# Optimization experiments

Measured on AMD Instinct MI355X. Metric: run time of the kernel, lower is better.

## Reference

```python
import jax, jax.numpy as jnp
import numpy as np

B, T, I, H, C, S, V = 32, 64, 300, 168, 168, 512, 50257


def setup_inputs() -> dict:
    key = jax.random.key(0)
    ks = jax.random.split(key, 10)
    s = 0.05
    return {
        "x": jax.random.normal(ks[0], (B, T, I), jnp.float32),
        "context": jax.random.normal(ks[1], (B, S, C), jnp.float32),
        "context_lengths": jax.random.randint(ks[2], (B,), 1, S + 1),
        "W_ih": jax.random.normal(ks[3], (4 * H, I + C), jnp.float32) * s,
        "W_hh": jax.random.normal(ks[4], (4 * H, H), jnp.float32) * s,
        "b_ih": jnp.zeros((4 * H,), jnp.float32),
        "b_hh": jnp.zeros((4 * H,), jnp.float32),
        "att_Wx": jax.random.normal(ks[5], (H, H), jnp.float32) * s,
        "att_Ws": jax.random.normal(ks[6], (C, H), jnp.float32) * s,
        "att_b": jnp.zeros((H,), jnp.float32),
        "att_v": jax.random.normal(ks[7], (H,), jnp.float32) * s,
        "W_dec": jax.random.normal(ks[8], (V, H), jnp.float32) * s,
    }


def reference(x, context, context_lengths, W_ih, W_hh, b_ih, b_hh,
              att_Wx, att_Ws, att_b, att_v, W_dec):
    # x: (B, T, I); context: (B, S, C)
    b, t, _ = x.shape
    s_len = context.shape[1]
    h_dim = W_hh.shape[1]
    dtype = x.dtype

    # valid-position mask for attention over source context
    mask = jnp.arange(s_len)[None, :] < context_lengths[:, None]  # (B, S)
    # seq projection is time-invariant: precompute once outside the step loop
    seq_proj = jnp.einsum('bsc,ca->bsa', context, att_Ws)  # (B, S, H)

    h0 = jnp.zeros((b, h_dim), dtype)
    c0 = jnp.zeros((b, h_dim), dtype)

    def step(carry, x_t):
        h, c = carry
        # MLP (additive) attention: v . tanh(Wx h + Ws seq + b)
        e = jnp.einsum('bsa,a->bs',
                       jnp.tanh((h @ att_Wx)[:, None, :] + seq_proj + att_b),
                       att_v)  # (B, S)
        e = jnp.where(mask, e, jnp.asarray(-1e9, dtype))
        w = jax.nn.softmax(e, axis=-1)
        attn_ctx = jnp.einsum('bs,bsc->bc', w, context)  # (B, C)

        # concat input with attended context, single-layer LSTM cell
        rnn_in = jnp.concatenate([x_t, attn_ctx], axis=1)  # (B, I+C)
        gates = rnn_in @ W_ih.T + b_ih + h @ W_hh.T + b_hh  # (B, 4H)
        i_g, f_g, g_g, o_g = jnp.split(gates, 4, axis=1)    # torch ifgo order
        c_new = jax.nn.sigmoid(f_g) * c + jax.nn.sigmoid(i_g) * jnp.tanh(g_g)
        h_new = jax.nn.sigmoid(o_g) * jnp.tanh(c_new)

        dec = h_new @ W_dec.T  # (B, V), bias-free decode
        return (h_new, c_new), dec

    _, decs = jax.lax.scan(step, (h0, c0), jnp.swapaxes(x, 0, 1))  # (T, B, V)
    return jnp.swapaxes(decs, 0, 1)  # (B, T, V)
```

## Files before the change

### kernel.cpp

```cpp
#include <hip/hip_runtime.h>
#include <stdint.h>

#define BB 32
#define TT 64
#define ID 300
#define HH 168
#define SS 512
#define VV 50257
#define G4 672
#define IC 468
#define KP 192
#define NP2 50432
#define NJ 8
#define RPB 21
#define CPB 84
#define KK 336
#define WKP 88
#define EPAD 170
#define SBLK 64
#define LSLOT 192
#define HROW 96
#define LP 72
#define NTN 197
#define NTILES 1576

typedef float f32x4 __attribute__((ext_vector_type(4)));
typedef short bf16x8 __attribute__((ext_vector_type(8)));
typedef unsigned long long u64;

__device__ __forceinline__ float bf2f(unsigned short u) {
  union { unsigned int i; float f; } v; v.i = ((unsigned int)u) << 16; return v.f;
}
__device__ __forceinline__ unsigned short f2bf(float f) {
  union { float f; unsigned int u; } v; v.f = f;
  unsigned int r = v.u + 0x7fffu + ((v.u >> 16) & 1u);
  return (unsigned short)(r >> 16);
}
__device__ __forceinline__ float rcpf(float x) { return __builtin_amdgcn_rcpf(x); }
__device__ __forceinline__ u64 packft(float f, unsigned tag) {
  union { float f; unsigned u; } v; v.f = f;
  return ((u64)tag << 32) | (u64)v.u;
}
__device__ __forceinline__ float lo_f(u64 x) {
  union { unsigned u; float f; } v; v.u = (unsigned)x; return v.f;
}
__device__ __forceinline__ unsigned hi_u(u64 x) { return (unsigned)(x >> 32); }
__device__ __forceinline__ void postv(u64* p, u64 v) {
  __hip_atomic_store(p, v, __ATOMIC_RELAXED, __HIP_MEMORY_SCOPE_AGENT);
}
__device__ __forceinline__ u64 loadv(const u64* p) {
  return __hip_atomic_load(p, __ATOMIC_RELAXED, __HIP_MEMORY_SCOPE_AGENT);
}
__device__ __forceinline__ void postu(unsigned* p, unsigned v) {
  __hip_atomic_store(p, v, __ATOMIC_RELAXED, __HIP_MEMORY_SCOPE_AGENT);
}
__device__ __forceinline__ unsigned loadu(const unsigned* p) {
  return __hip_atomic_load(p, __ATOMIC_RELAXED, __HIP_MEMORY_SCOPE_AGENT);
}

#define NB_WDEC 4728
#define NB_TR   788
__global__ void k_prepall(const float* __restrict__ Wih, const float* __restrict__ Whh,
                          const float* __restrict__ attWx, const float* __restrict__ Wd,
                          float* __restrict__ WihxT, unsigned short* __restrict__ Wdb,
                          float* __restrict__ WgT, unsigned short* __restrict__ WxS,
                          u64* __restrict__ Abuf, u64* __restrict__ Pbuf,
                          unsigned* __restrict__ pw) {
  const int bid = blockIdx.x, tid = threadIdx.x;
  if (bid < NB_WDEC) {
    size_t e0 = ((size_t)bid * 256 + tid) * 8;
    int v = (int)(e0 / KP), kp0 = (int)(e0 - (size_t)v * KP);
    int rg = kp0 / 24, off0 = kp0 - rg * 24;
    unsigned short o[8];
    if (v < VV) {
      const float* src = Wd + (size_t)v * HH + rg * RPB + off0;
      #pragma unroll
      for (int i = 0; i < 8; ++i) o[i] = (off0 + i < RPB) ? f2bf(src[i]) : 0;
    } else {
      #pragma unroll
      for (int i = 0; i < 8; ++i) o[i] = 0;
    }
    *(uint4*)(Wdb + e0) = *(const uint4*)o;
    return;
  }
  if (bid < NB_WDEC + NB_TR) {
    int idx = (bid - NB_WDEC) * 256 + tid;
    if (idx < ID * G4) {
      int k = idx / G4, i = idx - k * G4;
      WihxT[idx] = Wih[(size_t)i * IC + k];
    }
    return;
  }
  int idx = (bid - NB_WDEC - NB_TR) * 256 + tid;
  const int T1 = NJ * KK * WKP;
  const int T2 = T1 + NJ * RPB * HH;
  const int ZH = BB * NJ * LSLOT;
  const int T3 = T2 + 2 * ZH + 64;
  if (idx < T1) {
    int j = idx / (KK * WKP); int r = idx - j * (KK * WKP);
    int k = r / WKP, col = r - k * WKP;
    float w = 0.f;
    if (col < CPB) {
      int gt = col / RPB, rr = col - gt * RPB;
      int gcol = gt * HH + j * RPB + rr;
      w = (k < HH) ? Wih[(size_t)gcol * IC + ID + k] : Whh[(size_t)gcol * HH + (k - HH)];
    }
    WgT[idx] = w;
  } else if (idx < T2) {
    int r = idx - T1;
    WxS[r] = f2bf(attWx[r]);
  } else if (idx < T3) {
    int r = idx - T2;
    if (r < ZH) Abuf[r] = 0ull;
    else if (r < 2 * ZH) Pbuf[r - ZH] = 0ull;
    else pw[r - 2 * ZH] = 0u;
  }
}

__global__ void k_seqxp(const float* __restrict__ ctx, const float* __restrict__ Ws,
                        const float* __restrict__ x, const float* __restrict__ WihxT,
                        const float* __restrict__ bih, const float* __restrict__ bhh,
                        unsigned short* __restrict__ ETs, unsigned short* __restrict__ ctxb,
                        float* __restrict__ Xp) {
  __shared__ float sbuf[2688];
  const int tid = threadIdx.x;
  if (blockIdx.x < 1024) {
    const int b = blockIdx.x & 31;
    const int s0 = (blockIdx.x >> 5) * 16;
    for (int idx = tid; idx < 16 * HH; idx += 256) {
      float v = ctx[(size_t)(b * SS + s0) * HH + idx];
      sbuf[idx] = v;
      ctxb[(size_t)(b * SS + s0) * HH + idx] = f2bf(v);
    }
    __syncthreads();
    #pragma unroll
    for (int o = 0; o < 11; ++o) {
      int idx = o * 256 + tid;
      if (idx < 16 * HH) {
        int s = idx / HH, h = idx - s * HH;
        const float* cr = &sbuf[s * HH];
        float acc = 0.f;
        #pragma unroll 4
        for (int c = 0; c < HH; ++c) acc = fmaf(cr[c], Ws[c * HH + h], acc);
        ETs[(size_t)(b * SS + s0 + s) * HH + h] = f2bf(__expf(2.f * acc));
      }
    }
  } else {
    const int r = blockIdx.x - 1024;
    const int t0 = (r & 7) * 8;
    const int b = r >> 3;
    for (int idx = tid; idx < 8 * ID; idx += 256)
      sbuf[idx] = x[(size_t)(b * TT + t0) * ID + idx];
    __syncthreads();
    for (int i = tid; i < G4; i += 256) {
      float bias = bih[i] + bhh[i];
      float acc[8];
      #pragma unroll
      for (int tt = 0; tt < 8; ++tt) acc[tt] = bias;
      for (int k = 0; k < ID; ++k) {
        float w = WihxT[k * G4 + i];
        #pragma unroll
        for (int tt = 0; tt < 8; ++tt) acc[tt] += sbuf[tt * ID + k] * w;
      }
      #pragma unroll
      for (int tt = 0; tt < 8; ++tt)
        Xp[(size_t)(b * TT + t0 + tt) * G4 + i] = acc[tt];
    }
  }
}

__global__ __launch_bounds__(512, 1) void k_recur(
    const int* __restrict__ lens, const float* __restrict__ attb,
    const float* __restrict__ attv, const float* __restrict__ WgT,
    const unsigned short* __restrict__ WxS, const unsigned short* __restrict__ ETs,
    const unsigned short* __restrict__ ctxb, const float* __restrict__ Xp,
    u64* __restrict__ Abuf, u64* __restrict__ Pbuf,
    unsigned* __restrict__ hallA, const unsigned short* __restrict__ Wdb,
    float* __restrict__ out, unsigned* __restrict__ pw) {
  const int b = blockIdx.x & 31;
  const int j = blockIdx.x >> 5;
  const int tid = threadIdx.x;

  __shared__ __align__(16) float WgL[KK][WKP];
  __shared__ unsigned short EL[SBLK][EPAD];
  __shared__ unsigned short WxL[RPB][HH];
  __shared__ float scratch[512];
  __shared__ float redH[504], redC[504];
  __shared__ float gE[HH], hsh[HH], abL[HH], vL[HH], attn[HH];
  __shared__ float esh[SBLK], hLoc[RPB], cLoc[RPB], wsum[8];
  __shared__ float sumv_s, bsum_s;
  __shared__ int sClaim;

  {
    const f32x4* src = (const f32x4*)(WgT + (size_t)j * KK * WKP);
    f32x4* dst = (f32x4*)WgL;
    for (int i = tid; i < KK * WKP / 4; i += 512) dst[i] = src[i];
  }
  for (int i = tid; i < SBLK * HH; i += 512) {
    int s = i / HH, h = i - s * HH;
    EL[s][h] = ETs[((size_t)b * SS + j * SBLK + s) * HH + h];
  }
  for (int i = tid; i < RPB * HH; i += 512)
    ((unsigned short*)WxL)[i] = WxS[(size_t)j * RPB * HH + i];
  if (tid < HH) { abL[tid] = attb[tid]; vL[tid] = attv[tid]; }
  if (tid < RPB) cLoc[tid] = 0.f;
  __syncthreads();
  if (tid == 0) {
    float s = 0.f;
    for (int h = 0; h < HH; ++h) s += vL[h];
    sumv_s = s;
  }
  const int len = lens[b];
  const int sbase = j * SBLK;
  u64* Amine = Abuf + (size_t)(b * NJ + j) * LSLOT;
  u64* Pmine = Pbuf + (size_t)(b * NJ + j) * LSLOT;
  __syncthreads();

  for (int t = 0; t < TT; ++t) {
    float xa0=0,xa1=0,xa2=0,xa3=0, xb0=0,xb1=0,xb2=0,xb3=0;
    if (tid < 11) {
      const float* xp = Xp + ((size_t)b * TT + t) * G4 + j * RPB;
      int r0 = 2 * tid, r1 = r0 + 1;
      xa0 = xp[r0]; xa1 = xp[HH + r0]; xa2 = xp[2*HH + r0]; xa3 = xp[3*HH + r0];
      if (r1 < RPB) { xb0 = xp[r1]; xb1 = xp[HH + r1]; xb2 = xp[2*HH + r1]; xb3 = xp[3*HH + r1]; }
    }
    if (tid < HH) {
      float a = abL[tid], hv = 0.f;
      if (t > 0) {
        const unsigned want = (unsigned)t;
        const int jh = tid / RPB, hr = tid - jh * RPB;
        u64 va[9];
        int g = 0;
        for (;;) {
          #pragma unroll
          for (int jj = 0; jj < NJ; ++jj)
            va[jj] = loadv(&Abuf[(size_t)(b * NJ + jj) * LSLOT + tid]);
          va[8] = loadv(&Abuf[(size_t)(b * NJ + jh) * LSLOT + HH + hr]);
          bool ok = true;
          #pragma unroll
          for (int q = 0; q < 9; ++q) ok &= (hi_u(va[q]) >= want);
          if (ok) break;
          __builtin_amdgcn_s_sleep(1);
          if (++g > (1 << 24)) break;
        }
        #pragma unroll
        for (int jj = 0; jj < NJ; ++jj) a += lo_f(va[jj]);
        hv = lo_f(va[8]);
      }
      gE[tid] = __expf(2.f * a);
      hsh[tid] = hv;
    }
    __syncthreads();
    {
      int w = tid >> 6, lane = tid & 63;
      int sl = w * 8 + (lane >> 3);
      int hg = lane & 7;
      const unsigned short* er = &EL[sl][hg * RPB];
      const int hb = hg * RPB;
      float ep = 0.f;
      #pragma unroll 7
      for (int i = 0; i < RPB; ++i)
        ep += vL[hb + i] * rcpf(fmaf(gE[hb + i], bf2f(er[i]), 1.f));
      ep += __shfl_xor(ep, 1); ep += __shfl_xor(ep, 2); ep += __shfl_xor(ep, 4);
      float eh = (sbase + sl < len) ? __expf(sumv_s - 2.f * ep) : 0.f;
      float ws = (hg == 0) ? eh : 0.f;
      ws += __shfl_xor(ws, 8); ws += __shfl_xor(ws, 16); ws += __shfl_xor(ws, 32);
      if (lane == 0) wsum[w] = ws;
      if (hg == 0) esh[sl] = eh;
    }
    __syncthreads();
    if (tid < 504) {
      int c = tid % HH, ch = tid / HH;
      const unsigned short* cb = ctxb + ((size_t)b * SS + sbase) * HH + c;
      float p = 0.f;
      for (int s = ch; s < SBLK; s += 3)
        p = fmaf(esh[s], bf2f(cb[(size_t)s * HH]), p);
      scratch[ch * HH + c] = p;
    } else if (tid == 504) {
      float bs = 0.f;
      #pragma unroll
      for (int w = 0; w < 8; ++w) bs += wsum[w];
      bsum_s = bs;
    }
    __syncthreads();
    if (tid < HH) {
      float p = scratch[tid] + scratch[HH + tid] + scratch[2 * HH + tid];
      postv(&Pmine[tid], packft(p, (unsigned)(t + 1)));
    } else if (tid == HH) {
      postv(&Pmine[HH], packft(bsum_s, (unsigned)(t + 1)));
    }
    if (tid < 504) {
      int col = tid % CPB, kc = tid / CPB;
      int k0 = HH + kc * 28;
      float acc = 0.f;
      #pragma unroll 7
      for (int i = 0; i < 28; ++i)
        acc = fmaf(WgL[k0 + i][col], hsh[kc * 28 + i], acc);
      redH[kc * CPB + col] = acc;
    }
    if (tid < HH) {
      const unsigned want = (unsigned)(t + 1);
      u64 pv[NJ], bv[NJ];
      int g = 0;
      for (;;) {
        #pragma unroll
        for (int jj = 0; jj < NJ; ++jj) {
          const u64* pb = Pbuf + (size_t)(b * NJ + jj) * LSLOT;
          pv[jj] = loadv(&pb[tid]);
          bv[jj] = loadv(&pb[HH]);
        }
        bool ok = true;
        #pragma unroll
        for (int jj = 0; jj < NJ; ++jj) ok &= (hi_u(pv[jj]) >= want) & (hi_u(bv[jj]) >= want);
        if (ok) break;
        __builtin_amdgcn_s_sleep(1);
        if (++g > (1 << 24)) break;
      }
      float s = 0.f, den = 0.f;
      #pragma unroll
      for (int jj = 0; jj < NJ; ++jj) { s += lo_f(pv[jj]); den += lo_f(bv[jj]); }
      attn[tid] = s * rcpf(den);
    }
    __syncthreads();
    if (tid < 504) {
      int col = tid % CPB, kc = tid / CPB;
      int k0 = kc * 28;
      float acc = 0.f;
      #pragma unroll 7
      for (int i = 0; i < 28; ++i)
        acc = fmaf(WgL[k0 + i][col], attn[k0 + i], acc);
      redC[kc * CPB + col] = acc;
    }
    __syncthreads();
    if (tid < 12) {
      size_t hrow = ((size_t)b * TT + t) * HROW + j * 12;
      if (tid < 11) {
        const int r0 = 2 * tid, r1 = r0 + 1;
        float g0 = xa0, g1 = xa1, g2 = xa2, g3 = xa3;
        #pragma unroll
        for (int kc = 0; kc < 6; ++kc) {
          const float* rh = &redH[kc * CPB];
          const float* rc = &redC[kc * CPB];
          g0 += rh[r0] + rc[r0];
          g1 += rh[RPB + r0] + rc[RPB + r0];
          g2 += rh[2 * RPB + r0] + rc[2 * RPB + r0];
          g3 += rh[3 * RPB + r0] + rc[3 * RPB + r0];
        }
        float si = rcpf(1.f + __expf(-g0));
        float sf = rcpf(1.f + __expf(-g1));
        float tg = 1.f - 2.f * rcpf(1.f + __expf(2.f * g2));
        float so = rcpf(1.f + __expf(-g3));
        float cn = fmaf(sf, cLoc[r0], si * tg);
        float tc = 1.f - 2.f * rcpf(1.f + __expf(2.f * cn));
        float h0 = so * tc;
        cLoc[r0] = cn; hLoc[r0] = h0;
        unsigned hv = (unsigned)f2bf(h0);
        if (r1 < RPB) {
          float G0 = xb0, G1 = xb1, G2 = xb2, G3 = xb3;
          #pragma unroll
          for (int kc = 0; kc < 6; ++kc) {
            const float* rh = &redH[kc * CPB];
            const float* rc = &redC[kc * CPB];
            G0 += rh[r1] + rc[r1];
            G1 += rh[RPB + r1] + rc[RPB + r1];
            G2 += rh[2 * RPB + r1] + rc[2 * RPB + r1];
            G3 += rh[3 * RPB + r1] + rc[3 * RPB + r1];
          }
          float Si = rcpf(1.f + __expf(-G0));
          float Sf = rcpf(1.f + __expf(-G1));
          float Tg = 1.f - 2.f * rcpf(1.f + __expf(2.f * G2));
          float So = rcpf(1.f + __expf(-G3));
          float Cn = fmaf(Sf, cLoc[r1], Si * Tg);
          float Tc = 1.f - 2.f * rcpf(1.f + __expf(2.f * Cn));
          float h1 = So * Tc;
          cLoc[r1] = Cn; hLoc[r1] = h1;
          hv |= ((unsigned)f2bf(h1)) << 16;
        }
        postu(&hallA[hrow + tid], hv);
      } else {
        postu(&hallA[hrow + 11], 0u);
      }
    }
    __syncthreads();
    if (tid < HH) {
      float acc = 0.f;
      #pragma unroll
      for (int r = 0; r < RPB; ++r)
        acc = fmaf(hLoc[r], bf2f(WxL[r][tid]), acc);
      postv(&Amine[tid], packft(acc, (unsigned)(t + 1)));
    } else if (tid < HH + RPB) {
      postv(&Amine[tid], packft(hLoc[tid - HH], (unsigned)(t + 1)));
    }
  }

  __syncthreads();
  if (tid == 0) {
    __hip_atomic_fetch_add(&pw[0], 1u, __ATOMIC_RELAXED, __HIP_MEMORY_SCOPE_AGENT);
    int g = 0;
    while (loadu(&pw[0]) < (unsigned)(BB * NJ)) {
      __builtin_amdgcn_s_sleep(2);
      if (++g > (1 << 26)) break;
    }
  }
  __syncthreads();

  unsigned short* As = (unsigned short*)&WgL[0][0];
  unsigned short* Bs = As + 256 * LP;
  for (;;) {
    if (tid == 0) {
      unsigned w = __hip_atomic_fetch_add(&pw[32], 1u, __ATOMIC_RELAXED,
                                          __HIP_MEMORY_SCOPE_AGENT);
      sClaim = (w < NTILES) ? (int)w : -1;
    }
    __syncthreads();
    const int w = sClaim;
    if (w < 0) break;
    const int mt = w / NTN, nt = w - mt * NTN;
    const int m0 = mt * 256, n0 = nt * 256;
    const int lane = tid & 63, wid = tid >> 6;
    const int wm = wid >> 2, wn = wid & 3;
    const int lr = lane & 15, lk = lane >> 4;
    f32x4 acc[8][4];
    #pragma unroll
    for (int i = 0; i < 8; ++i)
      #pragma unroll
      for (int jj = 0; jj < 4; ++jj) acc[i][jj] = (f32x4)0.f;
    for (int k0 = 0; k0 < KP; k0 += 64) {
      if (k0) __syncthreads();
      #pragma unroll
      for (int i = 0; i < 4; ++i) {
        int flat = i * 512 + tid;
        int row = flat >> 3;
        int c8 = flat & 7;
        uint4 va = *(const uint4*)(hallA + (size_t)(m0 + row) * HROW + k0 / 2 + c8 * 4);
        *(uint4*)&As[row * LP + c8 * 8] = va;
        uint4 vb = *(const uint4*)(Wdb + (size_t)(n0 + row) * KP + k0 + c8 * 8);
        *(uint4*)&Bs[row * LP + c8 * 8] = vb;
      }
      __syncthreads();
      #pragma unroll
      for (int kk = 0; kk < 64; kk += 32) {
        bf16x8 af[8], bfr[4];
        #pragma unroll
        for (int mi = 0; mi < 8; ++mi)
          af[mi] = *(const bf16x8*)&As[(wm * 128 + mi * 16 + lr) * LP + kk + lk * 8];
        #pragma unroll
        for (int ni = 0; ni < 4; ++ni)
          bfr[ni] = *(const bf16x8*)&Bs[(wn * 64 + ni * 16 + lr) * LP + kk + lk * 8];
        #pragma unroll
        for (int mi = 0; mi < 8; ++mi)
          #pragma unroll
          for (int ni = 0; ni < 4; ++ni)
            acc[mi][ni] = __builtin_amdgcn_mfma_f32_16x16x32_bf16(
                af[mi], bfr[ni], acc[mi][ni], 0, 0, 0);
      }
    }
    #pragma unroll
    for (int mi = 0; mi < 8; ++mi)
      #pragma unroll
      for (int ni = 0; ni < 4; ++ni) {
        int col = n0 + wn * 64 + ni * 16 + lr;
        if (col < VV) {
          #pragma unroll
          for (int r = 0; r < 4; ++r) {
            int row = m0 + wm * 128 + mi * 16 + lk * 4 + r;
            out[(size_t)row * VV + col] = acc[mi][ni][r];
          }
        }
      }
    __syncthreads();
  }
}

extern "C" void kernel_launch(void* const* d_in, const int* in_sizes, int n_in,
                              void* d_out, int out_size, void* d_ws, size_t ws_size,
                              hipStream_t stream) {
  (void)in_sizes; (void)n_in; (void)out_size; (void)ws_size;
  const float* x     = (const float*)d_in[0];
  const float* ctx   = (const float*)d_in[1];
  const int*   lens  = (const int*)d_in[2];
  const float* Wih   = (const float*)d_in[3];
  const float* Whh   = (const float*)d_in[4];
  const float* bih   = (const float*)d_in[5];
  const float* bhh   = (const float*)d_in[6];
  const float* attWx = (const float*)d_in[7];
  const float* attWs = (const float*)d_in[8];
  const float* attb  = (const float*)d_in[9];
  const float* attv  = (const float*)d_in[10];
  const float* Wdec  = (const float*)d_in[11];
  float* out = (float*)d_out;

  char* base = (char*)d_ws;
  size_t off = 0;
  auto alloc = [&](size_t bytes) -> void* {
    off = (off + 255) & ~(size_t)255;
    void* p = base + off;
    off += bytes;
    return p;
  };
  unsigned short* ETs  = (unsigned short*)alloc((size_t)BB * SS * HH * 2);
  unsigned short* ctxb = (unsigned short*)alloc((size_t)BB * SS * HH * 2);
  float*          Xp   = (float*)alloc((size_t)BB * TT * G4 * 4);
  float*          WihxT= (float*)alloc((size_t)ID * G4 * 4);
  unsigned*       hallA= (unsigned*)alloc((size_t)BB * TT * HROW * 4);
  unsigned short* Wdb  = (unsigned short*)alloc((size_t)NP2 * KP * 2);
  float*          WgT  = (float*)alloc((size_t)NJ * KK * WKP * 4);
  unsigned short* WxS  = (unsigned short*)alloc((size_t)NJ * RPB * HH * 2);
  u64*            Abuf = (u64*)alloc((size_t)BB * NJ * LSLOT * 8);
  u64*            Pbuf = (u64*)alloc((size_t)BB * NJ * LSLOT * 8);
  unsigned*       pw   = (unsigned*)alloc(64 * 4);

  {
    const int TOTP = NJ * KK * WKP + NJ * RPB * HH + 2 * BB * NJ * LSLOT + 64;
    const int NBP = (TOTP + 255) / 256;
    k_prepall<<<dim3(NB_WDEC + NB_TR + NBP), dim3(256), 0, stream>>>(
        Wih, Whh, attWx, Wdec, WihxT, Wdb, WgT, WxS, Abuf, Pbuf, pw);
  }
  k_seqxp<<<dim3(1024 + 256), dim3(256), 0, stream>>>(ctx, attWs, x, WihxT,
                                                      bih, bhh, ETs, ctxb, Xp);
  {
    const int* a0 = lens; const float* a1 = attb; const float* a2 = attv;
    const float* a3 = WgT; const unsigned short* a4 = WxS;
    const unsigned short* a5 = ETs; const unsigned short* a6 = ctxb;
    const float* a7 = Xp; u64* a8 = Abuf; u64* a9 = Pbuf;
    unsigned* a10 = hallA; const unsigned short* a11 = Wdb;
    float* a12 = out; unsigned* a13 = pw;
    void* args[] = { &a0, &a1, &a2, &a3, &a4, &a5, &a6, &a7, &a8, &a9,
                     &a10, &a11, &a12, &a13 };
    hipLaunchCooperativeKernel((void*)k_recur, dim3(BB * NJ), dim3(512), args, 0, stream);
  }
}
```

Baseline: 834.2 us.

## Split decode GEMM into separate kernel and merge prep kernels

Moves the vocabulary decode GEMM out of the cooperative recurrent kernel, where 256 blocks claimed tiles from an atomic counter after a global barrier, into its own kernel launched over a 197x8 grid. The new kernel stages each output tile through shared memory so that global stores are row-contiguous. The two prep kernels are merged into one launch, and the Wih transpose is dropped in favour of reading Wih rows directly with vector loads. This adds a launch boundary between recurrence and decode but lets the decode use the whole GPU at full occupancy and removes the spin barrier.

```diff
diff --git a/kernel.cpp b/kernel.cpp
--- a/kernel.cpp
+++ b/kernel.cpp
@@ -22,7 +22,6 @@
 #define HROW 96
 #define LP 72
 #define NTN 197
-#define NTILES 1576
 
 typedef float f32x4 __attribute__((ext_vector_type(4)));
 typedef short bf16x8 __attribute__((ext_vector_type(8)));
@@ -54,19 +53,20 @@
 __device__ __forceinline__ void postu(unsigned* p, unsigned v) {
   __hip_atomic_store(p, v, __ATOMIC_RELAXED, __HIP_MEMORY_SCOPE_AGENT);
 }
-__device__ __forceinline__ unsigned loadu(const unsigned* p) {
-  return __hip_atomic_load(p, __ATOMIC_RELAXED, __HIP_MEMORY_SCOPE_AGENT);
-}
 
 #define NB_WDEC 4728
-#define NB_TR   788
-__global__ void k_prepall(const float* __restrict__ Wih, const float* __restrict__ Whh,
-                          const float* __restrict__ attWx, const float* __restrict__ Wd,
-                          float* __restrict__ WihxT, unsigned short* __restrict__ Wdb,
-                          float* __restrict__ WgT, unsigned short* __restrict__ WxS,
-                          u64* __restrict__ Abuf, u64* __restrict__ Pbuf,
-                          unsigned* __restrict__ pw) {
+#define NB_Z    1419
+__global__ void k_prep(const float* __restrict__ Wih, const float* __restrict__ Whh,
+                       const float* __restrict__ attWx, const float* __restrict__ Wd,
+                       const float* __restrict__ ctx, const float* __restrict__ attWs,
+                       const float* __restrict__ x, const float* __restrict__ bih,
+                       const float* __restrict__ bhh,
+                       unsigned short* __restrict__ Wdb, float* __restrict__ WgT,
+                       unsigned short* __restrict__ WxS, u64* __restrict__ Abuf,
+                       u64* __restrict__ Pbuf, unsigned short* __restrict__ ETs,
+                       unsigned short* __restrict__ ctxb, float* __restrict__ Xp) {
   const int bid = blockIdx.x, tid = threadIdx.x;
+  __shared__ float sbuf[2688];
   if (bid < NB_WDEC) {
     size_t e0 = ((size_t)bid * 256 + tid) * 8;
     int v = (int)(e0 / KP), kp0 = (int)(e0 - (size_t)v * KP);
@@ -83,50 +83,37 @@
     *(uint4*)(Wdb + e0) = *(const uint4*)o;
     return;
   }
-  if (bid < NB_WDEC + NB_TR) {
-    int idx = (bid - NB_WDEC) * 256 + tid;
-    if (idx < ID * G4) {
-      int k = idx / G4, i = idx - k * G4;
-      WihxT[idx] = Wih[(size_t)i * IC + k];
+  int b2 = bid - NB_WDEC;
+  if (b2 < NB_Z) {
+    int idx = b2 * 256 + tid;
+    const int T1 = NJ * KK * WKP;
+    const int T2 = T1 + NJ * RPB * HH;
+    const int ZH = BB * NJ * LSLOT;
+    const int T3 = T2 + 2 * ZH;
+    if (idx < T1) {
+      int j = idx / (KK * WKP); int r = idx - j * (KK * WKP);
+      int k = r / WKP, col = r - k * WKP;
+      float w = 0.f;
+      if (col < CPB) {
+        int gt = col / RPB, rr = col - gt * RPB;
+        int gcol = gt * HH + j * RPB + rr;
+        w = (k < HH) ? Wih[(size_t)gcol * IC + ID + k] : Whh[(size_t)gcol * HH + (k - HH)];
+      }
+      WgT[idx] = w;
+    } else if (idx < T2) {
+      int r = idx - T1;
+      WxS[r] = f2bf(attWx[r]);
+    } else if (idx < T3) {
+      int r = idx - T2;
+      if (r < ZH) Abuf[r] = 0ull;
+      else        Pbuf[r - ZH] = 0ull;
     }
     return;
   }
-  int idx = (bid - NB_WDEC - NB_TR) * 256 + tid;
-  const int T1 = NJ * KK * WKP;
-  const int T2 = T1 + NJ * RPB * HH;
-  const int ZH = BB * NJ * LSLOT;
-  const int T3 = T2 + 2 * ZH + 64;
-  if (idx < T1) {
-    int j = idx / (KK * WKP); int r = idx - j * (KK * WKP);
-    int k = r / WKP, col = r - k * WKP;
-    float w = 0.f;
-    if (col < CPB) {
-      int gt = col / RPB, rr = col - gt * RPB;
-      int gcol = gt * HH + j * RPB + rr;
-      w = (k < HH) ? Wih[(size_t)gcol * IC + ID + k] : Whh[(size_t)gcol * HH + (k - HH)];
-    }
-    WgT[idx] = w;
-  } else if (idx < T2) {
-    int r = idx - T1;
-    WxS[r] = f2bf(attWx[r]);
-  } else if (idx < T3) {
-    int r = idx - T2;
-    if (r < ZH) Abuf[r] = 0ull;
-    else if (r < 2 * ZH) Pbuf[r - ZH] = 0ull;
-    else pw[r - 2 * ZH] = 0u;
-  }
-}
-
-__global__ void k_seqxp(const float* __restrict__ ctx, const float* __restrict__ Ws,
-                        const float* __restrict__ x, const float* __restrict__ WihxT,
-                        const float* __restrict__ bih, const float* __restrict__ bhh,
-                        unsigned short* __restrict__ ETs, unsigned short* __restrict__ ctxb,
-                        float* __restrict__ Xp) {
-  __shared__ float sbuf[2688];
-  const int tid = threadIdx.x;
-  if (blockIdx.x < 1024) {
-    const int b = blockIdx.x & 31;
-    const int s0 = (blockIdx.x >> 5) * 16;
+  b2 -= NB_Z;
+  if (b2 < 1024) {
+    const int b = b2 & 31;
+    const int s0 = (b2 >> 5) * 16;
     for (int idx = tid; idx < 16 * HH; idx += 256) {
       float v = ctx[(size_t)(b * SS + s0) * HH + idx];
       sbuf[idx] = v;
@@ -141,14 +128,16 @@
         const float* cr = &sbuf[s * HH];
         float acc = 0.f;
         #pragma unroll 4
-        for (int c = 0; c < HH; ++c) acc = fmaf(cr[c], Ws[c * HH + h], acc);
+        for (int c = 0; c < HH; ++c) acc = fmaf(cr[c], attWs[c * HH + h], acc);
         ETs[(size_t)(b * SS + s0 + s) * HH + h] = f2bf(__expf(2.f * acc));
       }
     }
-  } else {
-    const int r = blockIdx.x - 1024;
-    const int t0 = (r & 7) * 8;
-    const int b = r >> 3;
+    return;
+  }
+  b2 -= 1024;
+  {
+    const int t0 = (b2 & 7) * 8;
+    const int b = b2 >> 3;
     for (int idx = tid; idx < 8 * ID; idx += 256)
       sbuf[idx] = x[(size_t)(b * TT + t0) * ID + idx];
     __syncthreads();
@@ -157,10 +146,14 @@
       float acc[8];
       #pragma unroll
       for (int tt = 0; tt < 8; ++tt) acc[tt] = bias;
-      for (int k = 0; k < ID; ++k) {
-        float w = WihxT[k * G4 + i];
-        #pragma unroll
-        for (int tt = 0; tt < 8; ++tt) acc[tt] += sbuf[tt * ID + k] * w;
+      const f32x4* wr = (const f32x4*)(Wih + (size_t)i * IC);
+      for (int k4 = 0; k4 < ID / 4; ++k4) {
+        f32x4 w = wr[k4];
+        #pragma unroll
+        for (int tt = 0; tt < 8; ++tt) {
+          const float* xr = &sbuf[tt * ID + k4 * 4];
+          acc[tt] += xr[0] * w[0] + xr[1] * w[1] + xr[2] * w[2] + xr[3] * w[3];
+        }
       }
       #pragma unroll
       for (int tt = 0; tt < 8; ++tt)
@@ -175,13 +168,12 @@
     const unsigned short* __restrict__ WxS, const unsigned short* __restrict__ ETs,
     const unsigned short* __restrict__ ctxb, const float* __restrict__ Xp,
     u64* __restrict__ Abuf, u64* __restrict__ Pbuf,
-    unsigned* __restrict__ hallA, const unsigned short* __restrict__ Wdb,
-    float* __restrict__ out, unsigned* __restrict__ pw) {
+    unsigned* __restrict__ hallA) {
   const int b = blockIdx.x & 31;
   const int j = blockIdx.x >> 5;
   const int tid = threadIdx.x;
 
-  __shared__ __align__(16) float WgL[KK][WKP];
+  __shared__ float WgL[KK][WKP];
   __shared__ unsigned short EL[SBLK][EPAD];
   __shared__ unsigned short WxL[RPB][HH];
   __shared__ float scratch[512];
@@ -189,7 +181,6 @@
   __shared__ float gE[HH], hsh[HH], abL[HH], vL[HH], attn[HH];
   __shared__ float esh[SBLK], hLoc[RPB], cLoc[RPB], wsum[8];
   __shared__ float sumv_s, bsum_s;
-  __shared__ int sClaim;
 
   {
     const f32x4* src = (const f32x4*)(WgT + (size_t)j * KK * WKP);
@@ -392,83 +383,84 @@
       postv(&Amine[tid], packft(hLoc[tid - HH], (unsigned)(t + 1)));
     }
   }
-
-  __syncthreads();
-  if (tid == 0) {
-    __hip_atomic_fetch_add(&pw[0], 1u, __ATOMIC_RELAXED, __HIP_MEMORY_SCOPE_AGENT);
-    int g = 0;
-    while (loadu(&pw[0]) < (unsigned)(BB * NJ)) {
-      __builtin_amdgcn_s_sleep(2);
-      if (++g > (1 << 26)) break;
-    }
-  }
-  __syncthreads();
-
-  unsigned short* As = (unsigned short*)&WgL[0][0];
-  unsigned short* Bs = As + 256 * LP;
-  for (;;) {
-    if (tid == 0) {
-      unsigned w = __hip_atomic_fetch_add(&pw[32], 1u, __ATOMIC_RELAXED,
-                                          __HIP_MEMORY_SCOPE_AGENT);
-      sClaim = (w < NTILES) ? (int)w : -1;
-    }
-    __syncthreads();
-    const int w = sClaim;
-    if (w < 0) break;
-    const int mt = w / NTN, nt = w - mt * NTN;
-    const int m0 = mt * 256, n0 = nt * 256;
-    const int lane = tid & 63, wid = tid >> 6;
-    const int wm = wid >> 2, wn = wid & 3;
-    const int lr = lane & 15, lk = lane >> 4;
-    f32x4 acc[8][4];
+}
+
+__global__ __launch_bounds__(512) void k_decode(const unsigned* __restrict__ hallA,
+                                                const unsigned short* __restrict__ wdb,
+                                                float* __restrict__ out) {
+  __shared__ __align__(16) unsigned short SM[2 * 256 * LP];
+  unsigned short* As = SM;
+  unsigned short* Bs = SM + 256 * LP;
+  const unsigned short* hallS = (const unsigned short*)hallA;
+  const int tid = threadIdx.x;
+  const int n0 = blockIdx.x * 256, m0 = blockIdx.y * 256;
+  const int lane = tid & 63, wid = tid >> 6;
+  const int wm = wid >> 2, wn = wid & 3;
+  const int lr = lane & 15, lk = lane >> 4;
+  f32x4 acc[8][4];
+  #pragma unroll
+  for (int i = 0; i < 8; ++i)
     #pragma unroll
-    for (int i = 0; i < 8; ++i)
-      #pragma unroll
-      for (int jj = 0; jj < 4; ++jj) acc[i][jj] = (f32x4)0.f;
-    for (int k0 = 0; k0 < KP; k0 += 64) {
-      if (k0) __syncthreads();
-      #pragma unroll
-      for (int i = 0; i < 4; ++i) {
-        int flat = i * 512 + tid;
-        int row = flat >> 3;
-        int c8 = flat & 7;
-        uint4 va = *(const uint4*)(hallA + (size_t)(m0 + row) * HROW + k0 / 2 + c8 * 4);
-        *(uint4*)&As[row * LP + c8 * 8] = va;
-        uint4 vb = *(const uint4*)(Wdb + (size_t)(n0 + row) * KP + k0 + c8 * 8);
-        *(uint4*)&Bs[row * LP + c8 * 8] = vb;
-      }
-      __syncthreads();
-      #pragma unroll
-      for (int kk = 0; kk < 64; kk += 32) {
-        bf16x8 af[8], bfr[4];
-        #pragma unroll
-        for (int mi = 0; mi < 8; ++mi)
-          af[mi] = *(const bf16x8*)&As[(wm * 128 + mi * 16 + lr) * LP + kk + lk * 8];
+    for (int jj = 0; jj < 4; ++jj) acc[i][jj] = (f32x4)0.f;
+
+  for (int k0 = 0; k0 < KP; k0 += 64) {
+    if (k0) __syncthreads();
+    #pragma unroll
+    for (int i = 0; i < 4; ++i) {
+      int flat = i * 512 + tid;
+      int row = flat >> 3;
+      int c8 = flat & 7;
+      uint4 va = *(const uint4*)(hallS + (size_t)(m0 + row) * KP + k0 + c8 * 8);
+      *(uint4*)&As[row * LP + c8 * 8] = va;
+      uint4 vb = *(const uint4*)(wdb + (size_t)(n0 + row) * KP + k0 + c8 * 8);
+      *(uint4*)&Bs[row * LP + c8 * 8] = vb;
+    }
+    __syncthreads();
+    #pragma unroll
+    for (int kk = 0; kk < 64; kk += 32) {
+      bf16x8 af[8], bfr[4];
+      #pragma unroll
+      for (int mi = 0; mi < 8; ++mi)
+        af[mi] = *(const bf16x8*)&As[(wm * 128 + mi * 16 + lr) * LP + kk + lk * 8];
+      #pragma unroll
+      for (int ni = 0; ni < 4; ++ni)
+        bfr[ni] = *(const bf16x8*)&Bs[(wn * 64 + ni * 16 + lr) * LP + kk + lk * 8];
+      #pragma unroll
+      for (int mi = 0; mi < 8; ++mi)
         #pragma unroll
         for (int ni = 0; ni < 4; ++ni)
-          bfr[ni] = *(const bf16x8*)&Bs[(wn * 64 + ni * 16 + lr) * LP + kk + lk * 8];
-        #pragma unroll
-        for (int mi = 0; mi < 8; ++mi)
-          #pragma unroll
-          for (int ni = 0; ni < 4; ++ni)
-            acc[mi][ni] = __builtin_amdgcn_mfma_f32_16x16x32_bf16(
-                af[mi], bfr[ni], acc[mi][ni], 0, 0, 0);
-      }
-    }
-    #pragma unroll
-    for (int mi = 0; mi < 8; ++mi)
-      #pragma unroll
-      for (int ni = 0; ni < 4; ++ni) {
-        int col = n0 + wn * 64 + ni * 16 + lr;
-        if (col < VV) {
+          acc[mi][ni] = __builtin_amdgcn_mfma_f32_16x16x32_bf16(
+              af[mi], bfr[ni], acc[mi][ni], 0, 0, 0);
+    }
+  }
+  float* Cl = (float*)SM;
+  for (int c = 0; c < 4; ++c) {
+    __syncthreads();
+    if (wm == (c >> 1)) {
+      const int mib = (c & 1) * 4;
+      #pragma unroll
+      for (int m2 = 0; m2 < 4; ++m2) {
+        #pragma unroll
+        for (int ni = 0; ni < 4; ++ni) {
           #pragma unroll
           for (int r = 0; r < 4; ++r) {
-            int row = m0 + wm * 128 + mi * 16 + lk * 4 + r;
-            out[(size_t)row * VV + col] = acc[mi][ni][r];
+            int lrow = m2 * 16 + lk * 4 + r;
+            Cl[lrow * 256 + wn * 64 + ni * 16 + lr] = acc[mib + m2][ni][r];
           }
         }
       }
-    __syncthreads();
+    }
+    __syncthreads();
+    const int rowbase = m0 + c * 64;
+    #pragma unroll
+    for (int q = 0; q < 32; ++q) {
+      int idx = q * 512 + tid;
+      int lrow = idx >> 8;
+      int cc = idx & 255;
+      int gcol = n0 + cc;
+      if (gcol < VV)
+        out[(size_t)(rowbase + lrow) * VV + gcol] = Cl[lrow * 256 + cc];
+    }
   }
 }
 
@@ -501,32 +493,24 @@
   unsigned short* ETs  = (unsigned short*)alloc((size_t)BB * SS * HH * 2);
   unsigned short* ctxb = (unsigned short*)alloc((size_t)BB * SS * HH * 2);
   float*          Xp   = (float*)alloc((size_t)BB * TT * G4 * 4);
-  float*          WihxT= (float*)alloc((size_t)ID * G4 * 4);
   unsigned*       hallA= (unsigned*)alloc((size_t)BB * TT * HROW * 4);
   unsigned short* Wdb  = (unsigned short*)alloc((size_t)NP2 * KP * 2);
   float*          WgT  = (float*)alloc((size_t)NJ * KK * WKP * 4);
   unsigned short* WxS  = (unsigned short*)alloc((size_t)NJ * RPB * HH * 2);
   u64*            Abuf = (u64*)alloc((size_t)BB * NJ * LSLOT * 8);
   u64*            Pbuf = (u64*)alloc((size_t)BB * NJ * LSLOT * 8);
-  unsigned*       pw   = (unsigned*)alloc(64 * 4);
-
-  {
-    const int TOTP = NJ * KK * WKP + NJ * RPB * HH + 2 * BB * NJ * LSLOT + 64;
-    const int NBP = (TOTP + 255) / 256;
-    k_prepall<<<dim3(NB_WDEC + NB_TR + NBP), dim3(256), 0, stream>>>(
-        Wih, Whh, attWx, Wdec, WihxT, Wdb, WgT, WxS, Abuf, Pbuf, pw);
-  }
-  k_seqxp<<<dim3(1024 + 256), dim3(256), 0, stream>>>(ctx, attWs, x, WihxT,
-                                                      bih, bhh, ETs, ctxb, Xp);
+
+  k_prep<<<dim3(NB_WDEC + NB_Z + 1024 + 256), dim3(256), 0, stream>>>(
+      Wih, Whh, attWx, Wdec, ctx, attWs, x, bih, bhh,
+      Wdb, WgT, WxS, Abuf, Pbuf, ETs, ctxb, Xp);
   {
     const int* a0 = lens; const float* a1 = attb; const float* a2 = attv;
     const float* a3 = WgT; const unsigned short* a4 = WxS;
     const unsigned short* a5 = ETs; const unsigned short* a6 = ctxb;
     const float* a7 = Xp; u64* a8 = Abuf; u64* a9 = Pbuf;
-    unsigned* a10 = hallA; const unsigned short* a11 = Wdb;
-    float* a12 = out; unsigned* a13 = pw;
-    void* args[] = { &a0, &a1, &a2, &a3, &a4, &a5, &a6, &a7, &a8, &a9,
-                     &a10, &a11, &a12, &a13 };
+    unsigned* a10 = hallA;
+    void* args[] = { &a0, &a1, &a2, &a3, &a4, &a5, &a6, &a7, &a8, &a9, &a10 };
     hipLaunchCooperativeKernel((void*)k_recur, dim3(BB * NJ), dim3(512), args, 0, stream);
   }
-}
+  k_decode<<<dim3(NTN, 8), dim3(512), 0, stream>>>(hallA, Wdb, out);
+}
```

Measured after the change: 878.8 us. 1.05x slower.
